# Kernel optimization log

Measured on AMD Instinct MI355X. Metric: run time of the kernel, lower is better.

## Reference

```python
import jax, jax.numpy as jnp
import numpy as np

C = 64
CK = C // 8  # query/key channels


def setup_inputs() -> dict:
    key = jax.random.key(0)
    ks = jax.random.split(key, 8)
    b, c, h, w = 4, C, 64, 64
    x = jax.random.normal(ks[0], (b, c, h, w), dtype=jnp.float32)
    # 1x1 conv weights (spectral-normalized weights are still just dense weights at eval)
    wq = jax.random.normal(ks[1], (CK, c), dtype=jnp.float32) * 0.05
    bq = jax.random.normal(ks[2], (CK,), dtype=jnp.float32) * 0.01
    wk = jax.random.normal(ks[3], (CK, c), dtype=jnp.float32) * 0.05
    bk = jax.random.normal(ks[4], (CK,), dtype=jnp.float32) * 0.01
    wv = jax.random.normal(ks[5], (c, c), dtype=jnp.float32) * 0.05
    bv = jax.random.normal(ks[6], (c,), dtype=jnp.float32) * 0.01
    # gamma is initialized to 0 in the module; use a nonzero value so the
    # attention path contributes to the output.
    gamma = jax.random.normal(ks[7], (1,), dtype=jnp.float32) * 0.5
    return {"x": x, "wq": wq, "bq": bq, "wk": wk, "bk": bk,
            "wv": wv, "bv": bv, "gamma": gamma}


def reference(x, wq, bq, wk, bk, wv, bv, gamma):
    b, c, h, w = x.shape
    n = h * w
    xf = x.reshape(b, c, n)                      # [b, c, n]
    # 1x1 convs as matmuls over the channel dim
    q = jnp.einsum('oc,bcn->bno', wq, xf) + bq   # [b, n, ck]
    k = jnp.einsum('oc,bcn->bon', wk, xf) + bk[None, :, None]  # [b, ck, n]
    v = jnp.einsum('oc,bcn->bno', wv, xf) + bv   # [b, n, c]
    attn = jax.nn.softmax(jnp.einsum('bnd,bdm->bnm', q, k), axis=-1)  # [b, n, n]
    o = jnp.einsum('bnm,bmc->bnc', attn, v)      # [b, n, c]
    o = o.transpose(0, 2, 1).reshape(b, c, h, w)
    return gamma[0] * o + x
```

## Files before the change

kernel.cpp:

```cpp
#include <hip/hip_runtime.h>

#define CH 64
#define NN 4096
#define NB 4
#define QT (NN / 16)
#define LOG2E 1.44269504f

typedef unsigned short u16;
typedef unsigned int u32;
typedef __attribute__((ext_vector_type(8))) short bf16x8;
typedef __attribute__((ext_vector_type(4))) float f32x4;

static __device__ __forceinline__ u16 bf16r(float f) {
  union { float f; unsigned u; } v; v.f = f;
  unsigned x = v.u;
  x += 0x7fffu + ((x >> 16) & 1u);
  return (u16)(x >> 16);
}
static __device__ __forceinline__ u32 pk2(float a, float b) {
  union { float f; unsigned u; } va, vb; va.f = a; vb.f = b;
  unsigned x = va.u, y = vb.u;
  x += 0x7fffu + ((x >> 16) & 1u);
  y += 0x7fffu + ((y >> 16) & 1u);
  return (x >> 16) | (y & 0xffff0000u);
}

__global__ __launch_bounds__(256) void qkv_proj(
    const float* __restrict__ x,
    const float* __restrict__ wq, const float* __restrict__ bq,
    const float* __restrict__ wk, const float* __restrict__ bk,
    const float* __restrict__ wv, const float* __restrict__ bv,
    u16* __restrict__ Qb, u16* __restrict__ Kb, u16* __restrict__ Vb) {
  __shared__ float wvs[64 * 64];
  __shared__ float wqs[8 * 64], wks[8 * 64];
  __shared__ float bvs[64], bqs[8], bks[8];
  const int t = threadIdx.x;
  for (int i = t; i < 64 * 64; i += 256) wvs[i] = wv[i];
  for (int i = t; i < 8 * 64; i += 256) { wqs[i] = wq[i]; wks[i] = wk[i]; }
  if (t < 64) bvs[t] = bv[t];
  if (t < 8) { bqs[t] = bq[t]; bks[t] = bk[t]; }
  __syncthreads();

  const int blk = blockIdx.x;
  const int b = blk >> 6;
  const int n0 = (blk & 63) << 6;
  const int p = t & 63;
  const int g = t >> 6;
  const float* xb = x + (size_t)b * CH * NN + n0 + p;

  float xr[64];
#pragma unroll
  for (int c = 0; c < 64; ++c) xr[c] = xb[(size_t)c * NN];

  const int k5 = p & 31;
  const int sperm = ((k5 & 15) >> 2) * 8 + (k5 & 3) + 4 * (k5 >> 4);
  const int nstore = n0 + (p & 32) + sperm;

  const int vch0 = g << 4;
  const size_t vbase = ((size_t)b * CH + vch0) * NN + nstore;
#pragma unroll
  for (int j = 0; j < 16; ++j) {
    const float4* wrow = reinterpret_cast<const float4*>(&wvs[(vch0 + j) * 64]);
    float s = 0.f;
#pragma unroll
    for (int c4 = 0; c4 < 16; ++c4) {
      float4 w = wrow[c4];
      s = fmaf(w.x, xr[4 * c4 + 0], s);
      s = fmaf(w.y, xr[4 * c4 + 1], s);
      s = fmaf(w.z, xr[4 * c4 + 2], s);
      s = fmaf(w.w, xr[4 * c4 + 3], s);
    }
    Vb[vbase + (size_t)j * NN] = bf16r(s + bvs[vch0 + j]);
  }

  if (g < 2) {
    const float* ws = (g == 0) ? wqs : wks;
    const float* bs = (g == 0) ? bqs : bks;
    float o[8];
#pragma unroll
    for (int j = 0; j < 8; ++j) {
      const float4* wrow = reinterpret_cast<const float4*>(&ws[j * 64]);
      float s = 0.f;
#pragma unroll
      for (int c4 = 0; c4 < 16; ++c4) {
        float4 w = wrow[c4];
        s = fmaf(w.x, xr[4 * c4 + 0], s);
        s = fmaf(w.y, xr[4 * c4 + 1], s);
        s = fmaf(w.z, xr[4 * c4 + 2], s);
        s = fmaf(w.w, xr[4 * c4 + 3], s);
      }
      s += bs[j];
      o[j] = (g == 0) ? s * (0.25f * LOG2E) : s;
    }
    uint4 pkv;
    pkv.x = pk2(o[0], o[1]); pkv.y = pk2(o[2], o[3]);
    pkv.z = pk2(o[4], o[5]); pkv.w = pk2(o[6], o[7]);
    u16* dst = ((g == 0) ? Qb : Kb) + ((size_t)b * NN + n0 + p) * 8;
    *reinterpret_cast<uint4*>(dst) = pkv;
  }
}

template <int PART>
__global__ __launch_bounds__(1024) void flash_attn(
    const float* __restrict__ x, const float* __restrict__ gamma,
    const u16* __restrict__ Qb, const u16* __restrict__ Kb,
    const u16* __restrict__ Vb, float* __restrict__ out,
    float* __restrict__ ACC, float* __restrict__ Lb,
    int klen, int nsplit) {
  __shared__ u16 Klds[2][64 * 8];
  __shared__ u16 Vlds[2][64 * 64];
  const int b = blockIdx.y, sp = blockIdx.z;
  const int w = __builtin_amdgcn_readfirstlane(threadIdx.x >> 6);
  const int lane = threadIdx.x & 63;
  const int q = lane & 15, g = lane >> 4;
  const int qrow0 = (blockIdx.x << 8) + (w << 4);
  const int ks = sp * klen;
  const int T = klen >> 6;

  bf16x8 qf = *reinterpret_cast<const bf16x8*>(
      Qb + ((size_t)b * NN + qrow0 + q) * 8);

  const u16* Kp = Kb + ((size_t)b * NN + ks) * 8;
  const u16* Vp = Vb + (size_t)b * CH * NN + ks;

  f32x4 acc[4] = {{0,0,0,0},{0,0,0,0},{0,0,0,0},{0,0,0,0}};
  const f32x4 zz = {0, 0, 0, 0};
  float lsum = 0.f;

  const int vrow = (w << 3) + (lane >> 3);
  const int vcp = lane & 7;
  const size_t vsrc = (size_t)vrow * NN + ((vcp ^ (vrow & 7)) << 3);

#define STAGE(tt, bb) do {                                                    \
    if (w < 8)                                                                \
      __builtin_amdgcn_global_load_lds(                                       \
          (const __attribute__((address_space(1))) void*)(Vp + vsrc + (tt) * 64), \
          (__attribute__((address_space(3))) void*)&Vlds[bb][w << 9], 16, 0, 0); \
    else if (w == 8)                                                          \
      __builtin_amdgcn_global_load_lds(                                       \
          (const __attribute__((address_space(1))) void*)(Kp + ((size_t)(tt) * 64 + lane) * 8), \
          (__attribute__((address_space(3))) void*)&Klds[bb][0], 16, 0, 0);   \
  } while (0)

  int buf = 0;
  STAGE(0, 0);

  for (int t = 0; t < T; ++t) {
    __syncthreads();
    if (t + 1 < T) STAGE(t + 1, buf ^ 1);
    const u16* Kl = &Klds[buf][0];
    const u16* Vl = &Vlds[buf][0];
#pragma unroll
    for (int grp = 0; grp < 2; ++grp) {
      bf16x8 kfA = *reinterpret_cast<const bf16x8*>(Kl + (grp * 32 + q) * 8);
      bf16x8 kfB = *reinterpret_cast<const bf16x8*>(Kl + (grp * 32 + 16 + q) * 8);
      f32x4 sA = __builtin_amdgcn_mfma_f32_16x16x32_bf16(kfA, qf, zz, 0, 0, 0);
      f32x4 sB = __builtin_amdgcn_mfma_f32_16x16x32_bf16(kfB, qf, zz, 0, 0, 0);
      float p0 = exp2f(sA[0]), p1 = exp2f(sA[1]);
      float p2 = exp2f(sA[2]), p3 = exp2f(sA[3]);
      float p4 = exp2f(sB[0]), p5 = exp2f(sB[1]);
      float p6 = exp2f(sB[2]), p7 = exp2f(sB[3]);
      lsum += ((p0 + p1) + (p2 + p3)) + ((p4 + p5) + (p6 + p7));
      union { uint4 u; bf16x8 v; } pb;
      pb.u.x = pk2(p0, p1); pb.u.y = pk2(p2, p3);
      pb.u.z = pk2(p4, p5); pb.u.w = pk2(p6, p7);
#pragma unroll
      for (int c = 0; c < 4; ++c) {
        const int row = c * 16 + q;
        bf16x8 vf = *reinterpret_cast<const bf16x8*>(
            Vl + row * 64 + ((((grp << 2) + g) ^ (q & 7)) << 3));
        acc[c] = __builtin_amdgcn_mfma_f32_16x16x32_bf16(vf, pb.v, acc[c], 0, 0, 0);
      }
    }
    buf ^= 1;
  }
#undef STAGE

  lsum += __shfl_xor(lsum, 16);
  lsum += __shfl_xor(lsum, 32);

  if (PART) {
    const int tile16 = (blockIdx.x << 4) + w;
    float* A = ACC + (size_t)((b * QT + tile16) * nsplit + sp) * 64 * 16;
#pragma unroll
    for (int c = 0; c < 4; ++c)
#pragma unroll
      for (int r = 0; r < 4; ++r)
        A[(size_t)(c * 16 + 4 * g + r) * 16 + q] = acc[c][r];
    if (g == 0)
      Lb[(size_t)((b * QT + tile16) * nsplit + sp) * 16 + q] = lsum;
  } else {
    const float gm = gamma[0] / lsum;
    const size_t obase = (size_t)b * CH * NN + qrow0 + q;
#pragma unroll
    for (int c = 0; c < 4; ++c)
#pragma unroll
      for (int r = 0; r < 4; ++r) {
        size_t i = obase + (size_t)(c * 16 + 4 * g + r) * NN;
        out[i] = fmaf(gm, acc[c][r], x[i]);
      }
  }
}

__global__ __launch_bounds__(256) void combine(
    const float* __restrict__ x, const float* __restrict__ gamma,
    const float* __restrict__ ACC, const float* __restrict__ Lb,
    float* __restrict__ out, int nsplit) {
  const int idx = blockIdx.x * 256 + threadIdx.x;
  const int n = idx & (NN - 1);
  const int ch = (idx >> 12) & 63;
  const int b = idx >> 18;
  const int tl = b * QT + (n >> 4);
  const int q = n & 15;
  float a = 0.f, l = 0.f;
  for (int s = 0; s < nsplit; ++s) {
    a += ACC[((size_t)(tl * nsplit + s) * 64 + ch) * 16 + q];
    l += Lb[(size_t)(tl * nsplit + s) * 16 + q];
  }
  out[idx] = fmaf(a, gamma[0] / l, x[idx]);
}

extern "C" void kernel_launch(void* const* d_in, const int* in_sizes, int n_in,
                              void* d_out, int out_size, void* d_ws, size_t ws_size,
                              hipStream_t stream) {
  const float* x     = (const float*)d_in[0];
  const float* wq    = (const float*)d_in[1];
  const float* bq    = (const float*)d_in[2];
  const float* wk    = (const float*)d_in[3];
  const float* bk    = (const float*)d_in[4];
  const float* wv    = (const float*)d_in[5];
  const float* bv    = (const float*)d_in[6];
  const float* gamma = (const float*)d_in[7];
  float* out = (float*)d_out;

  u16* Qb = (u16*)d_ws;
  u16* Kb = Qb + (size_t)NB * NN * 8;
  u16* Vb = Kb + (size_t)NB * NN * 8;
  float* ACC = (float*)(Vb + (size_t)NB * CH * NN);
  const size_t qkv_bytes = ((size_t)NB * NN * 8 * 2 + (size_t)NB * CH * NN) * 2;
  const size_t tiles = (size_t)NB * QT;

  int S = 0;
  for (int c : {4, 2, 1}) {
    size_t need = qkv_bytes + tiles * (size_t)c * (64 * 16 + 16) * 4;
    if (ws_size >= need) { S = c; break; }
  }

  qkv_proj<<<dim3(NB * (NN / 64)), dim3(256), 0, stream>>>(
      x, wq, bq, wk, bk, wv, bv, Qb, Kb, Vb);

  if (S > 1) {
    float* Lbuf = ACC + tiles * (size_t)S * 64 * 16;
    flash_attn<1><<<dim3(NN / 256, NB, S), dim3(1024), 0, stream>>>(
        x, gamma, Qb, Kb, Vb, out, ACC, Lbuf, NN / S, S);
    combine<<<dim3((NB * CH * NN) / 256), dim3(256), 0, stream>>>(
        x, gamma, ACC, Lbuf, out, S);
  } else {
    flash_attn<0><<<dim3(NN / 256, NB, 1), dim3(1024), 0, stream>>>(
        x, gamma, Qb, Kb, Vb, out, nullptr, nullptr, NN, 1);
  }
}
```

Baseline: 121.8 us.

## Switch attention to 32x32 MFMA tiles with fixed 8-way key split and bf16 partials

Rewrites the flash-attention kernel to use 32x32x16 bf16 MFMA with 128-key tiles, 512-thread blocks and a fixed 8-way key split. Partial accumulators are stored packed as bf16 pairs, and the combine kernel reads them back. The goal is higher matrix-core throughput, more parallelism, and less partial-output traffic. Separately, it removes the spurious 0.25 query scale and adjusts the V store permutation for the new layout. Risks include precision loss from bf16 partials and a larger fixed workspace requirement.

```diff
diff --git a/kernel.cpp b/kernel.cpp
--- a/kernel.cpp
+++ b/kernel.cpp
@@ -3,13 +3,17 @@
 #define CH 64
 #define NN 4096
 #define NB 4
-#define QT (NN / 16)
+#define SPLIT 8
+#define KLEN (NN / SPLIT)
+#define KTILE 128
+#define NT (KLEN / KTILE)
+#define QBLK 256
 #define LOG2E 1.44269504f
 
 typedef unsigned short u16;
 typedef unsigned int u32;
 typedef __attribute__((ext_vector_type(8))) short bf16x8;
-typedef __attribute__((ext_vector_type(4))) float f32x4;
+typedef __attribute__((ext_vector_type(16))) float f32x16;
 
 static __device__ __forceinline__ u16 bf16r(float f) {
   union { float f; unsigned u; } v; v.f = f;
@@ -53,7 +57,7 @@
   for (int c = 0; c < 64; ++c) xr[c] = xb[(size_t)c * NN];
 
   const int k5 = p & 31;
-  const int sperm = ((k5 & 15) >> 2) * 8 + (k5 & 3) + 4 * (k5 >> 4);
+  const int sperm = (k5 & 19) | ((k5 & 4) << 1) | ((k5 & 8) >> 1);
   const int nstore = n0 + (p & 32) + sperm;
 
   const int vch0 = g << 4;
@@ -90,7 +94,7 @@
         s = fmaf(w.w, xr[4 * c4 + 3], s);
       }
       s += bs[j];
-      o[j] = (g == 0) ? s * (0.25f * LOG2E) : s;
+      o[j] = (g == 0) ? s * LOG2E : s;
     }
     uint4 pkv;
     pkv.x = pk2(o[0], o[1]); pkv.y = pk2(o[2], o[3]);
@@ -100,124 +104,130 @@
   }
 }
 
-template <int PART>
-__global__ __launch_bounds__(1024) void flash_attn(
-    const float* __restrict__ x, const float* __restrict__ gamma,
+__global__ __launch_bounds__(512, 4) void flash_attn(
     const u16* __restrict__ Qb, const u16* __restrict__ Kb,
-    const u16* __restrict__ Vb, float* __restrict__ out,
-    float* __restrict__ ACC, float* __restrict__ Lb,
-    int klen, int nsplit) {
-  __shared__ u16 Klds[2][64 * 8];
-  __shared__ u16 Vlds[2][64 * 64];
+    const u16* __restrict__ Vb, u32* __restrict__ ACCu,
+    float* __restrict__ Lb) {
+  __shared__ u16 Klds[2][1032];
+  __shared__ u16 Vlds[2][8192];
   const int b = blockIdx.y, sp = blockIdx.z;
   const int w = __builtin_amdgcn_readfirstlane(threadIdx.x >> 6);
   const int lane = threadIdx.x & 63;
-  const int q = lane & 15, g = lane >> 4;
-  const int qrow0 = (blockIdx.x << 8) + (w << 4);
-  const int ks = sp * klen;
-  const int T = klen >> 6;
-
-  bf16x8 qf = *reinterpret_cast<const bf16x8*>(
-      Qb + ((size_t)b * NN + qrow0 + q) * 8);
+  const int l31 = lane & 31;
+  const int h = lane >> 5;
+  const int x7 = l31 & 7;
+  const int qrow0 = blockIdx.x * QBLK + w * 32;
+  const int ks = sp * KLEN;
+
+  if (threadIdx.x < 8) {
+    Klds[0][1024 + threadIdx.x] = 0;
+    Klds[1][1024 + threadIdx.x] = 0;
+  }
+
+  bf16x8 qf = {0, 0, 0, 0, 0, 0, 0, 0};
+  if (h == 0)
+    qf = *reinterpret_cast<const bf16x8*>(Qb + ((size_t)b * NN + qrow0 + l31) * 8);
 
   const u16* Kp = Kb + ((size_t)b * NN + ks) * 8;
   const u16* Vp = Vb + (size_t)b * CH * NN + ks;
 
-  f32x4 acc[4] = {{0,0,0,0},{0,0,0,0},{0,0,0,0},{0,0,0,0}};
-  const f32x4 zz = {0, 0, 0, 0};
+  const int c15 = lane & 15;
+  const int vch0 = w * 8 + (lane >> 4);
+  const int vch1 = vch0 + 4;
+  const size_t vsrc0 = (size_t)vch0 * NN + (size_t)(((c15 & 8) | ((c15 ^ vch0) & 7)) * 8);
+  const size_t vsrc1 = (size_t)vch1 * NN + (size_t)(((c15 & 8) | ((c15 ^ vch1) & 7)) * 8);
+
+#define STAGE(tt, bb) do {                                                    \
+    __builtin_amdgcn_global_load_lds(                                         \
+        (const __attribute__((address_space(1))) void*)(Vp + vsrc0 + (tt) * KTILE), \
+        (__attribute__((address_space(3))) void*)&Vlds[bb][w * 1024], 16, 0, 0); \
+    __builtin_amdgcn_global_load_lds(                                         \
+        (const __attribute__((address_space(1))) void*)(Vp + vsrc1 + (tt) * KTILE), \
+        (__attribute__((address_space(3))) void*)&Vlds[bb][w * 1024 + 512], 16, 0, 0); \
+    if (w < 2)                                                                \
+      __builtin_amdgcn_global_load_lds(                                       \
+          (const __attribute__((address_space(1))) void*)(Kp + ((size_t)(tt) * KTILE + w * 64 + lane) * 8), \
+          (__attribute__((address_space(3))) void*)&Klds[bb][w * 512], 16, 0, 0); \
+  } while (0)
+
+  f32x16 acc0 = {}, acc1 = {};
+  const f32x16 zz = {};
   float lsum = 0.f;
 
-  const int vrow = (w << 3) + (lane >> 3);
-  const int vcp = lane & 7;
-  const size_t vsrc = (size_t)vrow * NN + ((vcp ^ (vrow & 7)) << 3);
-
-#define STAGE(tt, bb) do {                                                    \
-    if (w < 8)                                                                \
-      __builtin_amdgcn_global_load_lds(                                       \
-          (const __attribute__((address_space(1))) void*)(Vp + vsrc + (tt) * 64), \
-          (__attribute__((address_space(3))) void*)&Vlds[bb][w << 9], 16, 0, 0); \
-    else if (w == 8)                                                          \
-      __builtin_amdgcn_global_load_lds(                                       \
-          (const __attribute__((address_space(1))) void*)(Kp + ((size_t)(tt) * 64 + lane) * 8), \
-          (__attribute__((address_space(3))) void*)&Klds[bb][0], 16, 0, 0);   \
-  } while (0)
-
-  int buf = 0;
   STAGE(0, 0);
-
-  for (int t = 0; t < T; ++t) {
+#pragma unroll
+  for (int t = 0; t < NT; ++t) {
+    const int buf = t & 1;
     __syncthreads();
-    if (t + 1 < T) STAGE(t + 1, buf ^ 1);
+    if (t + 1 < NT) STAGE(t + 1, buf ^ 1);
     const u16* Kl = &Klds[buf][0];
     const u16* Vl = &Vlds[buf][0];
 #pragma unroll
-    for (int grp = 0; grp < 2; ++grp) {
-      bf16x8 kfA = *reinterpret_cast<const bf16x8*>(Kl + (grp * 32 + q) * 8);
-      bf16x8 kfB = *reinterpret_cast<const bf16x8*>(Kl + (grp * 32 + 16 + q) * 8);
-      f32x4 sA = __builtin_amdgcn_mfma_f32_16x16x32_bf16(kfA, qf, zz, 0, 0, 0);
-      f32x4 sB = __builtin_amdgcn_mfma_f32_16x16x32_bf16(kfB, qf, zz, 0, 0, 0);
-      float p0 = exp2f(sA[0]), p1 = exp2f(sA[1]);
-      float p2 = exp2f(sA[2]), p3 = exp2f(sA[3]);
-      float p4 = exp2f(sB[0]), p5 = exp2f(sB[1]);
-      float p6 = exp2f(sB[2]), p7 = exp2f(sB[3]);
-      lsum += ((p0 + p1) + (p2 + p3)) + ((p4 + p5) + (p6 + p7));
-      union { uint4 u; bf16x8 v; } pb;
-      pb.u.x = pk2(p0, p1); pb.u.y = pk2(p2, p3);
-      pb.u.z = pk2(p4, p5); pb.u.w = pk2(p6, p7);
-#pragma unroll
-      for (int c = 0; c < 4; ++c) {
-        const int row = c * 16 + q;
-        bf16x8 vf = *reinterpret_cast<const bf16x8*>(
-            Vl + row * 64 + ((((grp << 2) + g) ^ (q & 7)) << 3));
-        acc[c] = __builtin_amdgcn_mfma_f32_16x16x32_bf16(vf, pb.v, acc[c], 0, 0, 0);
-      }
+    for (int k32 = 0; k32 < 4; ++k32) {
+      const int kaddr = h ? 1024 : (k32 * 32 + l31) * 8;
+      bf16x8 kf = *reinterpret_cast<const bf16x8*>(Kl + kaddr);
+      f32x16 s = __builtin_amdgcn_mfma_f32_32x32x16_bf16(kf, qf, zz, 0, 0, 0);
+      float p[16];
+#pragma unroll
+      for (int r = 0; r < 16; ++r) { p[r] = exp2f(s[r]); lsum += p[r]; }
+      union { uint4 u; bf16x8 v; } pb0, pb1;
+      pb0.u.x = pk2(p[0], p[1]);   pb0.u.y = pk2(p[2], p[3]);
+      pb0.u.z = pk2(p[4], p[5]);   pb0.u.w = pk2(p[6], p[7]);
+      pb1.u.x = pk2(p[8], p[9]);   pb1.u.y = pk2(p[10], p[11]);
+      pb1.u.z = pk2(p[12], p[13]); pb1.u.w = pk2(p[14], p[15]);
+      const int c16_0 = k32 * 4 + h;
+      const int c16_1 = c16_0 + 2;
+      const int cp0 = (c16_0 & 8) | ((c16_0 ^ x7) & 7);
+      const int cp1 = (c16_1 & 8) | ((c16_1 ^ x7) & 7);
+      bf16x8 v00 = *reinterpret_cast<const bf16x8*>(Vl + l31 * 128 + cp0 * 8);
+      bf16x8 v01 = *reinterpret_cast<const bf16x8*>(Vl + l31 * 128 + cp1 * 8);
+      bf16x8 v10 = *reinterpret_cast<const bf16x8*>(Vl + (32 + l31) * 128 + cp0 * 8);
+      bf16x8 v11 = *reinterpret_cast<const bf16x8*>(Vl + (32 + l31) * 128 + cp1 * 8);
+      acc0 = __builtin_amdgcn_mfma_f32_32x32x16_bf16(v00, pb0.v, acc0, 0, 0, 0);
+      acc0 = __builtin_amdgcn_mfma_f32_32x32x16_bf16(v01, pb1.v, acc0, 0, 0, 0);
+      acc1 = __builtin_amdgcn_mfma_f32_32x32x16_bf16(v10, pb0.v, acc1, 0, 0, 0);
+      acc1 = __builtin_amdgcn_mfma_f32_32x32x16_bf16(v11, pb1.v, acc1, 0, 0, 0);
     }
-    buf ^= 1;
   }
 #undef STAGE
 
-  lsum += __shfl_xor(lsum, 16);
   lsum += __shfl_xor(lsum, 32);
 
-  if (PART) {
-    const int tile16 = (blockIdx.x << 4) + w;
-    float* A = ACC + (size_t)((b * QT + tile16) * nsplit + sp) * 64 * 16;
-#pragma unroll
-    for (int c = 0; c < 4; ++c)
-#pragma unroll
-      for (int r = 0; r < 4; ++r)
-        A[(size_t)(c * 16 + 4 * g + r) * 16 + q] = acc[c][r];
-    if (g == 0)
-      Lb[(size_t)((b * QT + tile16) * nsplit + sp) * 16 + q] = lsum;
-  } else {
-    const float gm = gamma[0] / lsum;
-    const size_t obase = (size_t)b * CH * NN + qrow0 + q;
-#pragma unroll
-    for (int c = 0; c < 4; ++c)
-#pragma unroll
-      for (int r = 0; r < 4; ++r) {
-        size_t i = obase + (size_t)(c * 16 + 4 * g + r) * NN;
-        out[i] = fmaf(gm, acc[c][r], x[i]);
-      }
-  }
+  const int gtile = b * (NN / 32) + blockIdx.x * 8 + w;
+  u32* A = ACCu + ((size_t)gtile * SPLIT + sp) * 32 * 32;
+#pragma unroll
+  for (int rp = 0; rp < 8; ++rp) {
+    const int chp = (rp & 1) + 4 * (rp >> 1) + 2 * h;
+    A[chp * 32 + l31]        = pk2(acc0[2 * rp], acc0[2 * rp + 1]);
+    A[(16 + chp) * 32 + l31] = pk2(acc1[2 * rp], acc1[2 * rp + 1]);
+  }
+  if (h == 0)
+    Lb[((size_t)gtile * SPLIT + sp) * 32 + l31] = lsum;
 }
 
 __global__ __launch_bounds__(256) void combine(
     const float* __restrict__ x, const float* __restrict__ gamma,
-    const float* __restrict__ ACC, const float* __restrict__ Lb,
-    float* __restrict__ out, int nsplit) {
+    const u32* __restrict__ ACCu, const float* __restrict__ Lb,
+    float* __restrict__ out) {
   const int idx = blockIdx.x * 256 + threadIdx.x;
   const int n = idx & (NN - 1);
-  const int ch = (idx >> 12) & 63;
-  const int b = idx >> 18;
-  const int tl = b * QT + (n >> 4);
-  const int q = n & 15;
-  float a = 0.f, l = 0.f;
-  for (int s = 0; s < nsplit; ++s) {
-    a += ACC[((size_t)(tl * nsplit + s) * 64 + ch) * 16 + q];
-    l += Lb[(size_t)(tl * nsplit + s) * 16 + q];
-  }
-  out[idx] = fmaf(a, gamma[0] / l, x[idx]);
+  const int cp = (idx >> 12) & 31;
+  const int b = idx >> 17;
+  const int gtile = b * (NN / 32) + (n >> 5);
+  const int q = n & 31;
+  float s0 = 0.f, s1 = 0.f, l = 0.f;
+#pragma unroll
+  for (int sp = 0; sp < SPLIT; ++sp) {
+    const u32 v = ACCu[(((size_t)gtile * SPLIT + sp) * 32 + cp) * 32 + q];
+    union { u32 u; float f; } lo, hi;
+    lo.u = v << 16; hi.u = v & 0xffff0000u;
+    s0 += lo.f; s1 += hi.f;
+    l += Lb[((size_t)gtile * SPLIT + sp) * 32 + q];
+  }
+  const float inv = gamma[0] / l;
+  const size_t i0 = ((size_t)b * CH + 2 * cp) * NN + n;
+  out[i0] = fmaf(inv, s0, x[i0]);
+  out[i0 + NN] = fmaf(inv, s1, x[i0 + NN]);
 }
 
 extern "C" void kernel_launch(void* const* d_in, const int* in_sizes, int n_in,
@@ -236,27 +246,13 @@
   u16* Qb = (u16*)d_ws;
   u16* Kb = Qb + (size_t)NB * NN * 8;
   u16* Vb = Kb + (size_t)NB * NN * 8;
-  float* ACC = (float*)(Vb + (size_t)NB * CH * NN);
-  const size_t qkv_bytes = ((size_t)NB * NN * 8 * 2 + (size_t)NB * CH * NN) * 2;
-  const size_t tiles = (size_t)NB * QT;
-
-  int S = 0;
-  for (int c : {4, 2, 1}) {
-    size_t need = qkv_bytes + tiles * (size_t)c * (64 * 16 + 16) * 4;
-    if (ws_size >= need) { S = c; break; }
-  }
+  u32* ACCu = (u32*)(Vb + (size_t)NB * CH * NN);
+  float* Lb = (float*)(ACCu + (size_t)NB * (NN / 32) * SPLIT * 32 * 32);
 
   qkv_proj<<<dim3(NB * (NN / 64)), dim3(256), 0, stream>>>(
       x, wq, bq, wk, bk, wv, bv, Qb, Kb, Vb);
-
-  if (S > 1) {
-    float* Lbuf = ACC + tiles * (size_t)S * 64 * 16;
-    flash_attn<1><<<dim3(NN / 256, NB, S), dim3(1024), 0, stream>>>(
-        x, gamma, Qb, Kb, Vb, out, ACC, Lbuf, NN / S, S);
-    combine<<<dim3((NB * CH * NN) / 256), dim3(256), 0, stream>>>(
-        x, gamma, ACC, Lbuf, out, S);
-  } else {
-    flash_attn<0><<<dim3(NN / 256, NB, 1), dim3(1024), 0, stream>>>(
-        x, gamma, Qb, Kb, Vb, out, nullptr, nullptr, NN, 1);
-  }
-}
+  flash_attn<<<dim3(NN / QBLK, NB, SPLIT), dim3(512), 0, stream>>>(
+      Qb, Kb, Vb, ACCu, Lb);
+  combine<<<dim3((NB * 32 * NN) / 256), dim3(256), 0, stream>>>(
+      x, gamma, ACCu, Lb, out);
+}
```

Result: slower. 139.6 us (+14.7%).
